# Performance work log

Hardware: AMD Instinct MI355X
Metric: run time of the kernel (lower is better)

Reference implementation:

```python
import jax, jax.numpy as jnp
import numpy as np
from jax import lax

CHUNK = 512  # query-point chunk for pairwise point-triangle distance
EPS = 1e-12
LOSS_WEIGHT = 1.0


def closest_point_on_tri(p, a, b, c):
    """Closest point on triangle (a,b,c) to p. Broadcasts over leading dims; last dim = 3.
    Ericson, Real-Time Collision Detection, ch. 5.1.5."""
    ab = b - a
    ac = c - a
    ap = p - a
    d1 = (ab * ap).sum(-1)
    d2 = (ac * ap).sum(-1)
    bp = p - b
    d3 = (ab * bp).sum(-1)
    d4 = (ac * bp).sum(-1)
    cp_ = p - c
    d5 = (ab * cp_).sum(-1)
    d6 = (ac * cp_).sum(-1)
    va = d3 * d6 - d5 * d4
    vb = d5 * d2 - d1 * d6
    vc = d1 * d4 - d3 * d2
    # edge / interior parameters (denominators guarded; masks pick valid regions)
    v_ab = (d1 / jnp.maximum(d1 - d3, EPS))[..., None]
    w_ac = (d2 / jnp.maximum(d2 - d6, EPS))[..., None]
    w_bc = ((d4 - d3) / jnp.maximum((d4 - d3) + (d5 - d6), EPS))[..., None]
    denom = jnp.maximum(va + vb + vc, EPS)
    v_in = (vb / denom)[..., None]
    w_in = (vc / denom)[..., None]
    cond1 = ((d1 <= 0) & (d2 <= 0))[..., None]            # vertex a
    cond2 = ((d3 >= 0) & (d4 <= d3))[..., None]           # vertex b
    cond3 = ((d6 >= 0) & (d5 <= d6))[..., None]           # vertex c
    cond4 = ((vc <= 0) & (d1 >= 0) & (d3 <= 0))[..., None]  # edge ab
    cond5 = ((vb <= 0) & (d2 >= 0) & (d6 <= 0))[..., None]  # edge ac
    cond6 = ((va <= 0) & ((d4 - d3) >= 0) & ((d5 - d6) >= 0))[..., None]  # edge bc
    out = a + ab * v_in + ac * w_in                      # interior
    out = jnp.where(cond6, b + (c - b) * w_bc, out)
    out = jnp.where(cond5, a + ac * w_ac, out)
    out = jnp.where(cond4, a + ab * v_ab, out)
    out = jnp.where(cond3, c, out)
    out = jnp.where(cond2, b, out)
    out = jnp.where(cond1, a, out)
    return out


def nearest_points_on_mesh(points, verts, faces):
    """Exact nearest point on mesh surface for each query point.
    points: [P,3], verts: [V,3], faces: [F,3] int. Returns cp [P,3]."""
    ta = verts[faces[:, 0]]  # [F,3]
    tb = verts[faces[:, 1]]
    tc = verts[faces[:, 2]]

    def chunk_argmin(pc):  # pc: [CHUNK,3]
        cp = closest_point_on_tri(pc[:, None, :], ta[None], tb[None], tc[None])  # [C,F,3]
        d2 = ((pc[:, None, :] - cp) ** 2).sum(-1)  # [C,F]
        return jnp.argmin(d2, axis=1)

    P = points.shape[0]
    idx = lax.map(chunk_argmin, points.reshape(-1, CHUNK, 3)).reshape(P)
    cp = closest_point_on_tri(points, ta[idx], tb[idx], tc[idx])  # [P,3]
    return cp


def _per_batch_loss(points, verts, faces):
    cp = nearest_points_on_mesh(points, verts, faces)
    # torch.norm(resid, p=2) is the Frobenius norm of the whole [P,3] residual (scalar);
    # closest point is detached in the original autograd.Function usage.
    resid = points - lax.stop_gradient(cp)
    dist = jnp.sqrt((resid ** 2).sum())
    height = verts[:, 1].max() - verts[:, 1].min()  # bbox_3d[1]
    return dist / height


def setup_inputs() -> dict:
    key = jax.random.key(0)
    k1, k2, k3 = jax.random.split(key, 3)
    B, P, V, F = 2, 8192, 4098, 8192
    body_verts = jax.random.normal(k1, (B, P, 3), dtype=jnp.float32)
    mesh_verts = jax.random.normal(k2, (B, V, 3), dtype=jnp.float32)
    faces = jax.random.randint(k3, (B, F, 3), 0, V, dtype=jnp.int32)
    return {"body_verts": body_verts, "mesh_verts": mesh_verts, "faces": faces}


def reference(body_verts, mesh_verts, faces):
    losses = jax.vmap(_per_batch_loss)(body_verts, mesh_verts, faces)  # [B]
    return jnp.mean(losses) * LOSS_WEIGHT
```

## Files before the change

kernel.cpp:

```cpp
#include <hip/hip_runtime.h>

#define EPSF 1e-12f
constexpr int BB = 2;
constexpr int PP = 8192;
constexpr int VV = 4098;
constexpr int FF = 8192;

constexpr int SLOW_F4 = 5;
constexpr int NCONST = 22;
constexpr int PTS_PER_BLOCK = 1024;
constexpr int NSLICES = 128;
constexpr int CHUNK_T = FF / NSLICES;

typedef float f2 __attribute__((ext_vector_type(2)));

__device__ __forceinline__ f2 vfma(f2 a, f2 b, f2 c) {
#if __has_builtin(__builtin_elementwise_fma)
    return __builtin_elementwise_fma(a, b, c);
#else
    return (f2){fmaf(a.x, b.x, c.x), fmaf(a.y, b.y, c.y)};
#endif
}
__device__ __forceinline__ f2 vmin2(f2 a, f2 b) { return __builtin_elementwise_min(a, b); }
__device__ __forceinline__ f2 vmax2(f2 a, f2 b) { return __builtin_elementwise_max(a, b); }
__device__ __forceinline__ f2 bc(float s) { return (f2){s, s}; }
__device__ __forceinline__ f2 clamp01(f2 x) { return vmin2(vmax2(x, bc(0.0f)), bc(1.0f)); }

__device__ __forceinline__ unsigned int fkey(float f) {
    unsigned int u = __float_as_uint(f);
    return (u >> 31) ? ~u : (u | 0x80000000u);
}
__device__ __forceinline__ float funkey(unsigned int k) {
    unsigned int u = (k >> 31) ? (k ^ 0x80000000u) : ~k;
    return __uint_as_float(u);
}

__global__ __launch_bounds__(256) void precompute_kernel(
    const float* __restrict__ verts, const int* __restrict__ faces,
    float* __restrict__ pairrec, float4* __restrict__ slowrec,
    unsigned long long* __restrict__ mask, unsigned int* __restrict__ minD,
    float* __restrict__ sums, unsigned int* __restrict__ ykmin,
    unsigned int* __restrict__ ykmax)
{
    int idx = blockIdx.x * 256 + threadIdx.x;
    if (idx < BB) { sums[idx] = 0.0f; ykmin[idx] = 0xFFFFFFFFu; ykmax[idx] = 0u; }
    if (idx < BB * PP) minD[idx] = 0x7F800000u;
    if (idx >= BB * FF) return;

    int b = idx / FF;
    const float* vb = verts + (size_t)b * VV * 3;
    int i0 = faces[idx * 3 + 0];
    int i1 = faces[idx * 3 + 1];
    int i2 = faces[idx * 3 + 2];

    float ax = vb[i0*3+0], ay = vb[i0*3+1], az = vb[i0*3+2];
    float bx = vb[i1*3+0], by = vb[i1*3+1], bz = vb[i1*3+2];
    float cx = vb[i2*3+0], cy = vb[i2*3+1], cz = vb[i2*3+2];

    float abx = bx-ax, aby = by-ay, abz = bz-az;
    float acx = cx-ax, acy = cy-ay, acz = cz-az;
    float bcx = cx-bx, bcy = cy-by, bcz = cz-bz;

    {
        float4* t = slowrec + (size_t)idx * SLOW_F4;
        t[0] = make_float4(ax, ay, az, abx);
        t[1] = make_float4(bx, by, bz, aby);
        t[2] = make_float4(cx, cy, cz, abz);
        t[3] = make_float4(acx, acy, acz, bcx);
        t[4] = make_float4(bcy, bcz, 0.0f, 0.0f);
    }

    float nx = aby*acz - abz*acy;
    float ny = abz*acx - abx*acz;
    float nz = abx*acy - aby*acx;

    float ka1  = abx*ax + aby*ay + abz*az;
    float ka2  = acx*ax + acy*ay + acz*az;
    float aa   = ax*ax + ay*ay + az*az;
    float abac = abx*acx + aby*acy + abz*acz;

    float ab2 = abx*abx + aby*aby + abz*abz;
    float ac2 = acx*acx + acy*acy + acz*acz;
    float bc2 = bcx*bcx + bcy*bcy + bcz*bcz;
    float nn  = nx*nx + ny*ny + nz*nz;

    float inv_ab2 = 1.0f / fmaxf(ab2, EPSF);
    float inv_ac2 = 1.0f / fmaxf(ac2, EPSF);
    float inv_bc2 = 1.0f / fmaxf(bc2, EPSF);
    float inv_nn  = 1.0f / fmaxf(nn,  EPSF);

    bool slowtri = !((nn > 0.03f * (ab2 * ac2)) &&
                     (ab2 > 1e-4f) && (ac2 > 1e-4f) && (bc2 > 1e-4f));

    unsigned long long mb = __ballot(slowtri);
    if ((threadIdx.x & 63) == 0) mask[idx >> 6] = mb;

    float INF = __uint_as_float(0x7F800000u);
    float cvals[NCONST] = {
        abx, aby, abz, ka1,
        acx, acy, acz, ka2,
        ax,  ay,  az,  slowtri ? INF : aa,
        ab2, ac2, abac, bc2,
        ab2 - abac, inv_ab2, inv_ac2, inv_bc2,
        inv_nn, nn
    };
    float* pr = pairrec + (size_t)(idx >> 1) * (2 * NCONST) + (idx & 1);
#pragma unroll
    for (int c = 0; c < NCONST; ++c) pr[2*c] = cvals[c];
}

__device__ __forceinline__ float tri_d2(
    float px, float py, float pz,
    float4 R0, float4 R1, float4 R2, float4 R3, float4 R4)
{
#pragma clang fp contract(off)
    float ax = R0.x, ay = R0.y, az = R0.z;
    float bx = R1.x, by = R1.y, bz = R1.z;
    float cx = R2.x, cy = R2.y, cz = R2.z;
    float abx = R0.w, aby = R1.w, abz = R2.w;
    float acx = R3.x, acy = R3.y, acz = R3.z;
    float bcx = R3.w, bcy = R4.x, bcz = R4.y;

    float apx = px - ax, apy = py - ay, apz = pz - az;
    float d1 = (abx*apx + aby*apy) + abz*apz;
    float d2 = (acx*apx + acy*apy) + acz*apz;
    float bpx = px - bx, bpy = py - by, bpz = pz - bz;
    float d3 = (abx*bpx + aby*bpy) + abz*bpz;
    float d4 = (acx*bpx + acy*bpy) + acz*bpz;
    float cqx = px - cx, cqy = py - cy, cqz = pz - cz;
    float d5 = (abx*cqx + aby*cqy) + abz*cqz;
    float d6 = (acx*cqx + acy*cqy) + acz*cqz;

    float va = d3*d6 - d5*d4;
    float vb = d5*d2 - d1*d6;
    float vc = d1*d4 - d3*d2;
    float u43 = d4 - d3;
    float u56 = d5 - d6;

    bool c1 = (d1 <= 0.0f) && (d2 <= 0.0f);
    bool c2 = (d3 >= 0.0f) && (d4 <= d3);
    bool c3 = (d6 >= 0.0f) && (d5 <= d6);
    bool c4 = (vc <= 0.0f) && (d1 >= 0.0f) && (d3 <= 0.0f);
    bool c5 = (vb <= 0.0f) && (d2 >= 0.0f) && (d6 <= 0.0f);
    bool c6 = (va <= 0.0f) && (u43 >= 0.0f) && (u56 >= 0.0f);

    int reg = c1 ? 0 : (c2 ? 1 : (c3 ? 2 : (c4 ? 3 : (c5 ? 4 : (c6 ? 5 : 6)))));

    float denom = fmaxf((va + vb) + vc, EPSF);
    float den1 = (reg == 3) ? fmaxf(d1 - d3, EPSF)
               : (reg == 5) ? fmaxf(u43 + u56, EPSF)
               : (reg == 6) ? denom : 1.0f;
    float num1 = (reg == 3) ? d1
               : (reg == 5) ? u43
               : (reg == 6) ? vb : 0.0f;
    float den2 = (reg == 4) ? fmaxf(d2 - d6, EPSF)
               : (reg == 6) ? denom : 1.0f;
    float num2 = (reg == 4) ? d2
               : (reg == 6) ? vc : 0.0f;
    float s = num1 / den1;
    float t = num2 / den2;

    bool useB = (reg == 1) || (reg == 5);
    bool useC = (reg == 2);
    float basex = useB ? bx : (useC ? cx : ax);
    float basey = useB ? by : (useC ? cy : ay);
    float basez = useB ? bz : (useC ? cz : az);
    bool e1bc = (reg == 5);
    float e1x = e1bc ? bcx : abx;
    float e1y = e1bc ? bcy : aby;
    float e1z = e1bc ? bcz : abz;

    float cpx = (basex + e1x*s) + acx*t;
    float cpy = (basey + e1y*s) + acy*t;
    float cpz = (basez + e1z*s) + acz*t;
    float rx = px - cpx, ry = py - cpy, rz = pz - cpz;
    return (rx*rx + ry*ry) + rz*rz;
}

__global__ __launch_bounds__(256) void dist_kernel(
    const float* __restrict__ pts, const f2* __restrict__ pair,
    const float4* __restrict__ sa, const unsigned long long* __restrict__ mask,
    unsigned int* __restrict__ minD)
{
    const float INF = __uint_as_float(0x7F800000u);
    int tid   = threadIdx.x;
    int pg    = blockIdx.x;
    int slice = blockIdx.y;

    int b  = pg >> 3;
    int p0 = pg * PTS_PER_BLOCK + tid;

    f2 X[4], Y[4], Z[4], W[4], m[4];
#pragma unroll
    for (int k = 0; k < 4; ++k) {
        int p = p0 + k * 256;
        X[k] = bc(pts[p*3+0]); Y[k] = bc(pts[p*3+1]); Z[k] = bc(pts[p*3+2]);
        W[k] = vfma(X[k], X[k], vfma(Y[k], Y[k], Z[k] * Z[k]));
        m[k] = bc(INF);
    }

    int t0 = b * FF + slice * CHUNK_T;
    const f2* cb = pair + (size_t)(t0 >> 1) * NCONST;

    for (int tp = 0; tp < CHUNK_T / 2; ++tp) {
        const f2* c = cb + tp * NCONST;
        f2 abx=c[0], aby=c[1], abz=c[2], ka1=c[3];
        f2 acx=c[4], acy=c[5], acz=c[6], ka2=c[7];
        f2 ax=c[8],  ay=c[9],  az=c[10], aa=c[11];
        f2 ab2=c[12], ac2=c[13], abac=c[14], bc2=c[15];
        f2 kbc=c[16], iab2=c[17], iac2=c[18], ibc2=c[19];
        f2 inn=c[20], nn=c[21];

#pragma unroll
        for (int k = 0; k < 4; ++k) {
            f2 sab = vfma(abx, X[k], vfma(aby, Y[k], abz * Z[k]));
            f2 sac = vfma(acx, X[k], vfma(acy, Y[k], acz * Z[k]));
            f2 adp = vfma(ax,  X[k], vfma(ay,  Y[k], az  * Z[k]));

            f2 d1 = sab - ka1, d2 = sac - ka2;
            f2 ap2 = vfma(bc(-2.0f), adp, W[k]) + aa;
            f2 bp2 = vfma(bc(-2.0f), d1, ap2) + ab2;

            f2 sA = clamp01(d1 * iab2);
            f2 dAB = vfma(-sA, vfma(-sA, ab2, d1 + d1), ap2);
            f2 sC = clamp01(d2 * iac2);
            f2 dAC = vfma(-sC, vfma(-sC, ac2, d2 + d2), ap2);
            f2 u43 = (d2 - d1) + kbc;
            f2 sB = clamp01(u43 * ibc2);
            f2 dBC = vfma(-sB, vfma(-sB, bc2, u43 + u43), bp2);

            f2 v = vfma(ac2, d1, -(abac * d2));
            f2 w = vfma(ab2, d2, -(abac * d1));
            f2 s = v + w;
            f2 dprod = vfma(w, d2, v * d1);
            f2 dIN = vfma(-dprod, inn, ap2);
            f2 g = vmin2(vmin2(v, w), nn - s);
            f2 dI = vfma(vmin2(g, bc(0.0f)), bc(-1e30f), dIN);

            m[k] = vmin2(m[k], vmin2(vmin2(dAB, dAC), vmin2(dBC, dI)));
        }
    }

    unsigned long long bits = mask[t0 >> 6];
    while (bits) {
        int bit = __builtin_ctzll(bits);
        bits &= bits - 1;
        const float4* sb = sa + (size_t)(t0 + bit) * SLOW_F4;
        float4 S0 = sb[0], S1 = sb[1], S2 = sb[2], S3 = sb[3], S4 = sb[4];
#pragma unroll
        for (int k = 0; k < 4; ++k)
            m[k].x = fminf(m[k].x, tri_d2(X[k].x, Y[k].x, Z[k].x, S0, S1, S2, S3, S4));
    }

#pragma unroll
    for (int k = 0; k < 4; ++k) {
        float r = fminf(m[k].x, m[k].y);
        atomicMin(&minD[p0 + k*256], __float_as_uint(fmaxf(r, 0.0f)));
    }
}

__global__ __launch_bounds__(256) void reduce1_kernel(
    const unsigned int* __restrict__ minD, const float* __restrict__ verts,
    float* __restrict__ sums, unsigned int* __restrict__ ykmin,
    unsigned int* __restrict__ ykmax)
{
    int blk = blockIdx.x;
    int b = blk >> 3, part = blk & 7;
    int tid = threadIdx.x;

    float s = 0.0f;
    int i0 = part * (PP / 8), i1 = i0 + (PP / 8);
    for (int i = i0 + tid; i < i1; i += 256)
        s += __uint_as_float(minD[b * PP + i]);

    float ymin = 3.4e38f, ymax = -3.4e38f;
    int v0 = part * 513, v1 = min(v0 + 513, VV);
    for (int i = v0 + tid; i < v1; i += 256) {
        float y = verts[((size_t)b * VV + i) * 3 + 1];
        ymin = fminf(ymin, y); ymax = fmaxf(ymax, y);
    }

    for (int off = 32; off > 0; off >>= 1) {
        s += __shfl_down(s, off);
        ymin = fminf(ymin, __shfl_down(ymin, off));
        ymax = fmaxf(ymax, __shfl_down(ymax, off));
    }

    __shared__ float shs[4], shmn[4], shmx[4];
    if ((tid & 63) == 0) {
        int w = tid >> 6;
        shs[w] = s; shmn[w] = ymin; shmx[w] = ymax;
    }
    __syncthreads();
    if (tid == 0) {
        float tot = shs[0], mn = shmn[0], mx = shmx[0];
        for (int w = 1; w < 4; ++w) {
            tot += shs[w];
            mn = fminf(mn, shmn[w]);
            mx = fmaxf(mx, shmx[w]);
        }
        atomicAdd(&sums[b], tot);
        atomicMin(&ykmin[b], fkey(mn));
        atomicMax(&ykmax[b], fkey(mx));
    }
}

__global__ __launch_bounds__(64) void reduce2_kernel(
    const float* __restrict__ sums, const unsigned int* __restrict__ ykmin,
    const unsigned int* __restrict__ ykmax, float* __restrict__ out)
{
    if (threadIdx.x == 0) {
        float r = 0.0f;
        for (int b = 0; b < BB; ++b) {
            float h = funkey(ykmax[b]) - funkey(ykmin[b]);
            r += sqrtf(sums[b]) / h;
        }
        out[0] = r * 0.5f;
    }
}

extern "C" void kernel_launch(void* const* d_in, const int* in_sizes, int n_in,
                              void* d_out, int out_size, void* d_ws, size_t ws_size,
                              hipStream_t stream) {
    const float* pts   = (const float*)d_in[0];
    const float* verts = (const float*)d_in[1];
    const int*   faces = (const int*)d_in[2];
    float* out = (float*)d_out;

    char* w = (char*)d_ws;
    float* pairrec = (float*)w;
    w += (size_t)(BB * FF / 2) * (2 * NCONST) * sizeof(float);
    float4* slowrec = (float4*)w;
    w += (size_t)BB * FF * SLOW_F4 * sizeof(float4);
    unsigned long long* mask = (unsigned long long*)w;
    w += (size_t)(BB * FF / 64) * sizeof(unsigned long long);
    unsigned int* minD = (unsigned int*)w;
    w += (size_t)BB * PP * sizeof(unsigned int);
    float* sums = (float*)w;          w += BB * sizeof(float);
    unsigned int* ykmin = (unsigned int*)w; w += BB * sizeof(unsigned int);
    unsigned int* ykmax = (unsigned int*)w;

    precompute_kernel<<<(BB * FF + 255) / 256, 256, 0, stream>>>(
        verts, faces, pairrec, slowrec, mask, minD, sums, ykmin, ykmax);

    dim3 grid(BB * PP / PTS_PER_BLOCK, NSLICES);
    dist_kernel<<<grid, 256, 0, stream>>>(
        pts, (const f2*)pairrec, slowrec, mask, minD);

    reduce1_kernel<<<16, 256, 0, stream>>>(minD, verts, sums, ykmin, ykmax);
    reduce2_kernel<<<1, 64, 0, stream>>>(sums, ykmin, ykmax, out);
}
```

Before: 199.4 us.

## Software-pipeline triangle record loads and merge final reductions into one kernel

The inner triangle loop in dist_kernel now double-buffers its per-pair constant records, loading the next record while evaluating the current one, to hide global/L2 load latency behind the distance arithmetic. The loop is kept at unroll 1 and over-reads by one record, so the workspace is padded. Separately, the two reduction kernels are collapsed into a single 1024-thread-per-batch kernel that atomically adds each batch's contribution to the output, which removes one launch. This raises register pressure in dist_kernel, which could lower occupancy, and makes the output depend on atomic ordering.

```diff
diff --git a/kernel.cpp b/kernel.cpp
--- a/kernel.cpp
+++ b/kernel.cpp
@@ -26,24 +26,14 @@
 __device__ __forceinline__ f2 bc(float s) { return (f2){s, s}; }
 __device__ __forceinline__ f2 clamp01(f2 x) { return vmin2(vmax2(x, bc(0.0f)), bc(1.0f)); }
 
-__device__ __forceinline__ unsigned int fkey(float f) {
-    unsigned int u = __float_as_uint(f);
-    return (u >> 31) ? ~u : (u | 0x80000000u);
-}
-__device__ __forceinline__ float funkey(unsigned int k) {
-    unsigned int u = (k >> 31) ? (k ^ 0x80000000u) : ~k;
-    return __uint_as_float(u);
-}
-
 __global__ __launch_bounds__(256) void precompute_kernel(
     const float* __restrict__ verts, const int* __restrict__ faces,
     float* __restrict__ pairrec, float4* __restrict__ slowrec,
     unsigned long long* __restrict__ mask, unsigned int* __restrict__ minD,
-    float* __restrict__ sums, unsigned int* __restrict__ ykmin,
-    unsigned int* __restrict__ ykmax)
+    float* __restrict__ out)
 {
     int idx = blockIdx.x * 256 + threadIdx.x;
-    if (idx < BB) { sums[idx] = 0.0f; ykmin[idx] = 0xFFFFFFFFu; ykmax[idx] = 0u; }
+    if (idx == 0) out[0] = 0.0f;
     if (idx < BB * PP) minD[idx] = 0x7F800000u;
     if (idx >= BB * FF) return;
 
@@ -177,6 +167,55 @@
     return (rx*rx + ry*ry) + rz*rz;
 }
 
+struct Rec { f2 v[NCONST]; };
+
+__device__ __forceinline__ Rec loadRec(const f2* p) {
+    Rec r;
+#pragma unroll
+    for (int i = 0; i < NCONST; ++i) r.v[i] = p[i];
+    return r;
+}
+
+__device__ __forceinline__ void evalRec(
+    const Rec& r, const f2* X, const f2* Y, const f2* Z, const f2* W, f2* m)
+{
+    f2 abx=r.v[0], aby=r.v[1], abz=r.v[2], ka1=r.v[3];
+    f2 acx=r.v[4], acy=r.v[5], acz=r.v[6], ka2=r.v[7];
+    f2 ax=r.v[8],  ay=r.v[9],  az=r.v[10], aa=r.v[11];
+    f2 ab2=r.v[12], ac2=r.v[13], abac=r.v[14], bc2=r.v[15];
+    f2 kbc=r.v[16], iab2=r.v[17], iac2=r.v[18], ibc2=r.v[19];
+    f2 inn=r.v[20], nn=r.v[21];
+
+#pragma unroll
+    for (int k = 0; k < 4; ++k) {
+        f2 sab = vfma(abx, X[k], vfma(aby, Y[k], abz * Z[k]));
+        f2 sac = vfma(acx, X[k], vfma(acy, Y[k], acz * Z[k]));
+        f2 adp = vfma(ax,  X[k], vfma(ay,  Y[k], az  * Z[k]));
+
+        f2 d1 = sab - ka1, d2 = sac - ka2;
+        f2 ap2 = vfma(bc(-2.0f), adp, W[k]) + aa;
+        f2 bp2 = vfma(bc(-2.0f), d1, ap2) + ab2;
+
+        f2 sA = clamp01(d1 * iab2);
+        f2 dAB = vfma(-sA, vfma(-sA, ab2, d1 + d1), ap2);
+        f2 sC = clamp01(d2 * iac2);
+        f2 dAC = vfma(-sC, vfma(-sC, ac2, d2 + d2), ap2);
+        f2 u43 = (d2 - d1) + kbc;
+        f2 sB = clamp01(u43 * ibc2);
+        f2 dBC = vfma(-sB, vfma(-sB, bc2, u43 + u43), bp2);
+
+        f2 v = vfma(ac2, d1, -(abac * d2));
+        f2 w = vfma(ab2, d2, -(abac * d1));
+        f2 s = v + w;
+        f2 dprod = vfma(w, d2, v * d1);
+        f2 dIN = vfma(-dprod, inn, ap2);
+        f2 g = vmin2(vmin2(v, w), nn - s);
+        f2 dI = vfma(vmin2(g, bc(0.0f)), bc(-1e30f), dIN);
+
+        m[k] = vmin2(m[k], vmin2(vmin2(dAB, dAC), vmin2(dBC, dI)));
+    }
+}
+
 __global__ __launch_bounds__(256) void dist_kernel(
     const float* __restrict__ pts, const f2* __restrict__ pair,
     const float4* __restrict__ sa, const unsigned long long* __restrict__ mask,
@@ -202,43 +241,13 @@
     int t0 = b * FF + slice * CHUNK_T;
     const f2* cb = pair + (size_t)(t0 >> 1) * NCONST;
 
-    for (int tp = 0; tp < CHUNK_T / 2; ++tp) {
-        const f2* c = cb + tp * NCONST;
-        f2 abx=c[0], aby=c[1], abz=c[2], ka1=c[3];
-        f2 acx=c[4], acy=c[5], acz=c[6], ka2=c[7];
-        f2 ax=c[8],  ay=c[9],  az=c[10], aa=c[11];
-        f2 ab2=c[12], ac2=c[13], abac=c[14], bc2=c[15];
-        f2 kbc=c[16], iab2=c[17], iac2=c[18], ibc2=c[19];
-        f2 inn=c[20], nn=c[21];
-
-#pragma unroll
-        for (int k = 0; k < 4; ++k) {
-            f2 sab = vfma(abx, X[k], vfma(aby, Y[k], abz * Z[k]));
-            f2 sac = vfma(acx, X[k], vfma(acy, Y[k], acz * Z[k]));
-            f2 adp = vfma(ax,  X[k], vfma(ay,  Y[k], az  * Z[k]));
-
-            f2 d1 = sab - ka1, d2 = sac - ka2;
-            f2 ap2 = vfma(bc(-2.0f), adp, W[k]) + aa;
-            f2 bp2 = vfma(bc(-2.0f), d1, ap2) + ab2;
-
-            f2 sA = clamp01(d1 * iab2);
-            f2 dAB = vfma(-sA, vfma(-sA, ab2, d1 + d1), ap2);
-            f2 sC = clamp01(d2 * iac2);
-            f2 dAC = vfma(-sC, vfma(-sC, ac2, d2 + d2), ap2);
-            f2 u43 = (d2 - d1) + kbc;
-            f2 sB = clamp01(u43 * ibc2);
-            f2 dBC = vfma(-sB, vfma(-sB, bc2, u43 + u43), bp2);
-
-            f2 v = vfma(ac2, d1, -(abac * d2));
-            f2 w = vfma(ab2, d2, -(abac * d1));
-            f2 s = v + w;
-            f2 dprod = vfma(w, d2, v * d1);
-            f2 dIN = vfma(-dprod, inn, ap2);
-            f2 g = vmin2(vmin2(v, w), nn - s);
-            f2 dI = vfma(vmin2(g, bc(0.0f)), bc(-1e30f), dIN);
-
-            m[k] = vmin2(m[k], vmin2(vmin2(dAB, dAC), vmin2(dBC, dI)));
-        }
+    Rec A = loadRec(cb);
+#pragma unroll 1
+    for (int tp = 0; tp < CHUNK_T / 2; tp += 2) {
+        Rec Bx = loadRec(cb + (tp + 1) * NCONST);
+        evalRec(A, X, Y, Z, W, m);
+        A = loadRec(cb + (tp + 2) * NCONST);
+        evalRec(Bx, X, Y, Z, W, m);
     }
 
     unsigned long long bits = mask[t0 >> 6];
@@ -259,23 +268,19 @@
     }
 }
 
-__global__ __launch_bounds__(256) void reduce1_kernel(
+__global__ __launch_bounds__(1024) void reduce_kernel(
     const unsigned int* __restrict__ minD, const float* __restrict__ verts,
-    float* __restrict__ sums, unsigned int* __restrict__ ykmin,
-    unsigned int* __restrict__ ykmax)
-{
-    int blk = blockIdx.x;
-    int b = blk >> 3, part = blk & 7;
+    float* __restrict__ out)
+{
+    int b = blockIdx.x;
     int tid = threadIdx.x;
 
     float s = 0.0f;
-    int i0 = part * (PP / 8), i1 = i0 + (PP / 8);
-    for (int i = i0 + tid; i < i1; i += 256)
+    for (int i = tid; i < PP; i += 1024)
         s += __uint_as_float(minD[b * PP + i]);
 
     float ymin = 3.4e38f, ymax = -3.4e38f;
-    int v0 = part * 513, v1 = min(v0 + 513, VV);
-    for (int i = v0 + tid; i < v1; i += 256) {
+    for (int i = tid; i < VV; i += 1024) {
         float y = verts[((size_t)b * VV + i) * 3 + 1];
         ymin = fminf(ymin, y); ymax = fmaxf(ymax, y);
     }
@@ -286,7 +291,7 @@
         ymax = fmaxf(ymax, __shfl_down(ymax, off));
     }
 
-    __shared__ float shs[4], shmn[4], shmx[4];
+    __shared__ float shs[16], shmn[16], shmx[16];
     if ((tid & 63) == 0) {
         int w = tid >> 6;
         shs[w] = s; shmn[w] = ymin; shmx[w] = ymax;
@@ -294,28 +299,12 @@
     __syncthreads();
     if (tid == 0) {
         float tot = shs[0], mn = shmn[0], mx = shmx[0];
-        for (int w = 1; w < 4; ++w) {
+        for (int w = 1; w < 16; ++w) {
             tot += shs[w];
             mn = fminf(mn, shmn[w]);
             mx = fmaxf(mx, shmx[w]);
         }
-        atomicAdd(&sums[b], tot);
-        atomicMin(&ykmin[b], fkey(mn));
-        atomicMax(&ykmax[b], fkey(mx));
-    }
-}
-
-__global__ __launch_bounds__(64) void reduce2_kernel(
-    const float* __restrict__ sums, const unsigned int* __restrict__ ykmin,
-    const unsigned int* __restrict__ ykmax, float* __restrict__ out)
-{
-    if (threadIdx.x == 0) {
-        float r = 0.0f;
-        for (int b = 0; b < BB; ++b) {
-            float h = funkey(ykmax[b]) - funkey(ykmin[b]);
-            r += sqrtf(sums[b]) / h;
-        }
-        out[0] = r * 0.5f;
+        atomicAdd(out, 0.5f * sqrtf(tot) / (mx - mn));
     }
 }
 
@@ -329,24 +318,19 @@
 
     char* w = (char*)d_ws;
     float* pairrec = (float*)w;
-    w += (size_t)(BB * FF / 2) * (2 * NCONST) * sizeof(float);
+    w += ((size_t)(BB * FF / 2) + 2) * (2 * NCONST) * sizeof(float);
     float4* slowrec = (float4*)w;
     w += (size_t)BB * FF * SLOW_F4 * sizeof(float4);
     unsigned long long* mask = (unsigned long long*)w;
     w += (size_t)(BB * FF / 64) * sizeof(unsigned long long);
     unsigned int* minD = (unsigned int*)w;
-    w += (size_t)BB * PP * sizeof(unsigned int);
-    float* sums = (float*)w;          w += BB * sizeof(float);
-    unsigned int* ykmin = (unsigned int*)w; w += BB * sizeof(unsigned int);
-    unsigned int* ykmax = (unsigned int*)w;
 
     precompute_kernel<<<(BB * FF + 255) / 256, 256, 0, stream>>>(
-        verts, faces, pairrec, slowrec, mask, minD, sums, ykmin, ykmax);
+        verts, faces, pairrec, slowrec, mask, minD, out);
 
     dim3 grid(BB * PP / PTS_PER_BLOCK, NSLICES);
     dist_kernel<<<grid, 256, 0, stream>>>(
         pts, (const f2*)pairrec, slowrec, mask, minD);
 
-    reduce1_kernel<<<16, 256, 0, stream>>>(minD, verts, sums, ykmin, ykmax);
-    reduce2_kernel<<<1, 64, 0, stream>>>(sums, ykmin, ykmax, out);
-}
+    reduce_kernel<<<BB, 1024, 0, stream>>>(minD, verts, out);
+}
```

New measurement: 194.9 us (median of 2 runs). 2.2% less time.
